# Kernel optimization log

Measured on AMD Instinct MI355X. Metric: run time of the kernel, lower is better.

The kernel has to match this reference:

```python
import jax, jax.numpy as jnp
import numpy as np

C = 8.0  # RG-LRU temporal-gate constant (Griffin paper, c = 8)


def setup_inputs() -> dict:
    key = jax.random.key(0)
    ks = jax.random.split(key, 4)
    S, B, D = 2048, 8, 2048  # (seq_len, batch, width); batch_first=False layout
    s = 1.0 / np.sqrt(D).astype(np.float32)
    return {
        "x": jax.random.normal(ks[0], (S, B, D), jnp.float32),
        "h0": jnp.zeros((B, D), jnp.float32),
        "W_x": jax.random.normal(ks[1], (D, D), jnp.float32) * s,
        "b_x": jnp.zeros((D,), jnp.float32),
        "W_a": jax.random.normal(ks[2], (D, D), jnp.float32) * s,
        "b_a": jnp.zeros((D,), jnp.float32),
        "a_param": jax.random.uniform(ks[3], (D,), jnp.float32, 0.3, 1.0),
    }


def _rg_lru(x, h0, W_x, b_x, W_a, b_a, a_param):
    # x: (S, B, D) time-major. RG-LRU (Griffin/Hawk), num_heads=1 so the
    # block-diagonal gate projections are plain dense D->D linears.
    S = x.shape[0]
    gate_x = jax.nn.sigmoid(jnp.einsum("sbd,ed->sbe", x, W_x) + b_x)  # input gate
    gate_a = jax.nn.sigmoid(jnp.einsum("sbd,ed->sbe", x, W_a) + b_a)  # recurrence gate
    log_a = -C * gate_a * jax.nn.softplus(a_param)  # (S, B, D), log of decay in (0,1)
    a = jnp.exp(log_a)
    multiplier = jnp.sqrt(1.0 - jnp.exp(2.0 * log_a))  # sqrt(1 - a^2) normalizer
    # Reset at segment start (t == 0): multiplier -> 1, decay -> 0 (cache cleared).
    reset = (jnp.arange(S) == 0)[:, None, None]
    multiplier = jnp.where(reset, 1.0, multiplier)
    a = jnp.where(reset, 0.0, a)
    normed_x = x * gate_x * multiplier  # gated, variance-normalized input

    def step(h, inp):
        a_t, x_t = inp
        h = a_t * h + x_t  # diagonal linear recurrence
        return h, h

    hn, y = jax.lax.scan(step, h0, (a, normed_x))
    return y, hn  # y: (S, B, D) since batch_first=False; hn: (B, D)


def reference(x, h0, W_x, b_x, W_a, b_a, a_param):
    return _rg_lru(x, h0, W_x, b_x, W_a, b_a, a_param)
```

## Files before the change

kernel.cpp:

```cpp
#include <hip/hip_runtime.h>
#include <cstdint>

#define S_LEN 2048
#define B_SZ 8
#define D_DIM 2048
#define M_DIM (S_LEN * B_SZ)
#define CHAINS (B_SZ * D_DIM)
#define BK 64
#define KTILES (D_DIM / BK)

typedef __bf16 bf16;
typedef bf16 bf16x8 __attribute__((ext_vector_type(8)));
typedef bf16 bf16x4 __attribute__((ext_vector_type(4)));
typedef float f32x4 __attribute__((ext_vector_type(4)));

__device__ __forceinline__ void async_copy16(void* lds, const void* g) {
    __builtin_amdgcn_global_load_lds(
        (const __attribute__((address_space(1))) unsigned int*)g,
        (__attribute__((address_space(3))) unsigned int*)lds,
        16, 0, 0);
}

__global__ void k_convert(const float4* __restrict__ x,
                          const float4* __restrict__ wx,
                          const float4* __restrict__ wa,
                          bf16* __restrict__ xb,
                          bf16* __restrict__ wi) {
    const long NX4 = (long)M_DIM * D_DIM / 4;
    const long NW4 = (long)D_DIM * D_DIM / 4;
    const long total = NX4 + 2 * NW4;
    for (long i = (long)blockIdx.x * blockDim.x + threadIdx.x; i < total;
         i += (long)gridDim.x * blockDim.x) {
        float4 v;
        bf16* dst;
        if (i < NX4) {
            v = x[i];
            dst = xb + 4 * i;
        } else {
            long k = i - NX4;
            const int isA = k >= NW4;
            if (isA) k -= NW4;
            const long e = k >> 9;
            const long col4 = k & 511;
            const long drow = (e >> 4) * 32 + (isA ? 16 : 0) + (e & 15);
            v = (isA ? wa : wx)[k];
            dst = wi + (drow * 512 + col4) * 4;
        }
        bf16x4 o;
        o[0] = (bf16)v.x; o[1] = (bf16)v.y; o[2] = (bf16)v.z; o[3] = (bf16)v.w;
        *reinterpret_cast<bf16x4*>(dst) = o;
    }
}

__global__ void k_cvec(const float* __restrict__ ap, float* __restrict__ cv) {
    int e = blockIdx.x * blockDim.x + threadIdx.x;
    if (e < D_DIM) {
        float v = ap[e];
        cv[e] = -8.0f * log1pf(expf(v));
    }
}

__global__ __launch_bounds__(512, 2) void k_gemm(
    const bf16* __restrict__ xb,
    const bf16* __restrict__ wi,
    const float* __restrict__ x32,
    const float* __restrict__ bx,
    const float* __restrict__ ba,
    const float* __restrict__ cv,
    float* __restrict__ abuf,
    float* __restrict__ y)
{
    __shared__ __align__(16) char smem[131072];

    const int tid  = threadIdx.x;
    const int lane = tid & 63;
    const int w    = tid >> 6;
    const int wm   = w >> 2;
    const int wn   = w & 3;

    const int orig = blockIdx.x;
    const int wgid = (orig & 7) * 128 + (orig >> 3);
    const int m0 = (wgid & 63) * 256;
    const int e0 = (wgid >> 6) * 256;

    const int srow  = lane >> 3;
    const int swz16 = ((lane & 7) ^ srow) * 16;

    const char* gA = (const char*)xb;
    const char* gB = (const char*)wi;

#define STAGE_A(buf, kt) do {                                                  \
    const long kb_ = (long)(kt) * 128 + swz16;                                 \
    _Pragma("unroll")                                                          \
    for (int j_ = 0; j_ < 4; ++j_) {                                           \
        const int br_ = w * 32 + j_ * 8;                                       \
        async_copy16(smem + (buf) * 65536 + br_ * 128,                         \
                     gA + ((long)(m0 + br_ + srow) * 4096 + kb_));             \
    } } while (0)

#define STAGE_B(buf, kt) do {                                                  \
    const long kb_ = (long)(kt) * 128 + swz16;                                 \
    _Pragma("unroll")                                                          \
    for (int j_ = 0; j_ < 4; ++j_) {                                           \
        const int br_ = w * 32 + j_ * 8;                                       \
        async_copy16(smem + (buf) * 65536 + 32768 + br_ * 128,                 \
                     gB + ((long)(e0 + br_ + srow) * 4096 + kb_));             \
    } } while (0)

#define PHASE_MID() do {                                                       \
    __builtin_amdgcn_s_barrier();                                              \
    asm volatile("s_waitcnt lgkmcnt(0)" ::: "memory");                         \
    __builtin_amdgcn_sched_barrier(0);                                         \
    __builtin_amdgcn_s_setprio(1); } while (0)

#define PHASE_END() do {                                                       \
    __builtin_amdgcn_s_setprio(0);                                             \
    __builtin_amdgcn_s_barrier(); } while (0)

    f32x4 acc[8][4];
#pragma unroll
    for (int i = 0; i < 8; ++i)
#pragma unroll
        for (int j = 0; j < 4; ++j) acc[i][j] = (f32x4)(0.0f);

    STAGE_A(0, 0); STAGE_B(0, 0);
    asm volatile("s_waitcnt vmcnt(0)" ::: "memory");
    __builtin_amdgcn_s_barrier();

    const int rL = lane & 15;

    for (int kt = 0; kt < KTILES; ++kt) {
        const int c  = kt & 1;
        const int nb = 1 - c;
        char* sA = smem + c * 65536;
        char* sB = sA + 32768;
        const bool pf = (kt < KTILES - 1);

        bf16x8 af[4], bf[4];

#define LOAD_AF(ihalf, ks) do {                                                \
    _Pragma("unroll")                                                          \
    for (int i_ = 0; i_ < 4; ++i_) {                                           \
        const int r_ = wm * 128 + ((ihalf) * 4 + i_) * 16 + rL;                \
        const int ch_ = (((ks) * 4 + (lane >> 4)) ^ (r_ & 7)) * 16;            \
        af[i_] = *reinterpret_cast<const bf16x8*>(sA + r_ * 128 + ch_);        \
    } } while (0)

#define LOAD_BF(ks) do {                                                       \
    _Pragma("unroll")                                                          \
    for (int j_ = 0; j_ < 4; ++j_) {                                           \
        const int r_ = wn * 64 + j_ * 16 + rL;                                 \
        const int ch_ = (((ks) * 4 + (lane >> 4)) ^ (r_ & 7)) * 16;            \
        bf[j_] = *reinterpret_cast<const bf16x8*>(sB + r_ * 128 + ch_);        \
    } } while (0)

#define MFMA16(ihalf) do {                                                     \
    _Pragma("unroll")                                                          \
    for (int i_ = 0; i_ < 4; ++i_)                                             \
        _Pragma("unroll")                                                      \
        for (int j_ = 0; j_ < 4; ++j_)                                         \
            acc[(ihalf) * 4 + i_][j_] = __builtin_amdgcn_mfma_f32_16x16x32_bf16( \
                af[i_], bf[j_], acc[(ihalf) * 4 + i_][j_], 0, 0, 0);           \
    } while (0)

        LOAD_BF(0); LOAD_AF(0, 0);
        if (pf) STAGE_A(nb, kt + 1);
        PHASE_MID(); MFMA16(0); PHASE_END();

        LOAD_AF(1, 0);
        if (pf) STAGE_B(nb, kt + 1);
        PHASE_MID(); MFMA16(1); PHASE_END();

        LOAD_BF(1); LOAD_AF(0, 1);
        PHASE_MID(); MFMA16(0); PHASE_END();

        LOAD_AF(1, 1);
        PHASE_MID(); MFMA16(1);
        __builtin_amdgcn_s_setprio(0);
        if (pf) asm volatile("s_waitcnt vmcnt(0)" ::: "memory");
        __builtin_amdgcn_s_barrier();

#undef LOAD_AF
#undef LOAD_BF
#undef MFMA16
    }

#undef STAGE_A
#undef STAGE_B
#undef PHASE_MID
#undef PHASE_END

    const int rgrp = lane >> 4;
    const int chb  = (e0 + wn * 64) >> 1;
#pragma unroll
    for (int jj = 0; jj < 2; ++jj) {
        const int ch = chb + jj * 16 + rL;
        const float bxv = bx[ch];
        const float bav = ba[ch];
        const float cvv = cv[ch];
#pragma unroll
        for (int i = 0; i < 8; ++i) {
#pragma unroll
            for (int r = 0; r < 4; ++r) {
                const int m = m0 + wm * 128 + i * 16 + rgrp * 4 + r;
                const float zx = acc[i][2 * jj][r] + bxv;
                const float za = acc[i][2 * jj + 1][r] + bav;
                const float gx = 1.0f / (1.0f + __expf(-zx));
                const float ga = 1.0f / (1.0f + __expf(-za));
                const float la = cvv * ga;
                float a = __expf(la);
                float mult = sqrtf(fmaxf(1.0f - a * a, 0.0f));
                if (m < B_SZ) { a = 0.0f; mult = 1.0f; }
                const long o = (long)m * D_DIM + ch;
                const float xv = x32[o];
                abuf[o] = a;
                y[o] = xv * gx * mult;
            }
        }
    }
}

__global__ __launch_bounds__(64) void k_scan(
    const float* __restrict__ abuf,
    float* __restrict__ y,
    const float* __restrict__ h0,
    float* __restrict__ hn) {
    const int c = blockIdx.x * 64 + threadIdx.x;
    float h = h0[c];

    float av0[16], xv0[16], av1[16], xv1[16];
#pragma unroll
    for (int j = 0; j < 16; ++j) {
        const long o = (long)j * CHAINS + c;
        av0[j] = abuf[o];
        xv0[j] = y[o];
    }
    for (int g = 0; g < 128; g += 2) {
        const long base1 = ((long)(g + 1) * 16) * CHAINS + c;
        if (g + 1 < 128) {
#pragma unroll
            for (int j = 0; j < 16; ++j) {
                av1[j] = abuf[base1 + (long)j * CHAINS];
                xv1[j] = y[base1 + (long)j * CHAINS];
            }
        }
        const long base0 = ((long)g * 16) * CHAINS + c;
#pragma unroll
        for (int j = 0; j < 16; ++j) {
            h = fmaf(av0[j], h, xv0[j]);
            y[base0 + (long)j * CHAINS] = h;
        }
        const long base2 = ((long)(g + 2) * 16) * CHAINS + c;
        if (g + 2 < 128) {
#pragma unroll
            for (int j = 0; j < 16; ++j) {
                av0[j] = abuf[base2 + (long)j * CHAINS];
                xv0[j] = y[base2 + (long)j * CHAINS];
            }
        }
        if (g + 1 < 128) {
#pragma unroll
            for (int j = 0; j < 16; ++j) {
                h = fmaf(av1[j], h, xv1[j]);
                y[base1 + (long)j * CHAINS] = h;
            }
        }
    }
    hn[c] = h;
}

extern "C" void kernel_launch(void* const* d_in, const int* in_sizes, int n_in,
                              void* d_out, int out_size, void* d_ws, size_t ws_size,
                              hipStream_t stream) {
    const float* x  = (const float*)d_in[0];
    const float* h0 = (const float*)d_in[1];
    const float* Wx = (const float*)d_in[2];
    const float* bx = (const float*)d_in[3];
    const float* Wa = (const float*)d_in[4];
    const float* ba = (const float*)d_in[5];
    const float* ap = (const float*)d_in[6];
    float* out = (float*)d_out;

    char* ws = (char*)d_ws;
    bf16*  xb   = (bf16*)(ws);
    bf16*  wi   = (bf16*)(ws + 67108864L);
    float* cv   = (float*)(ws + 83886080L);
    float* abuf = (float*)(ws + 83894272L);

    float* y  = out;
    float* hn = out + (long)M_DIM * D_DIM;

    k_convert<<<dim3(2048), dim3(256), 0, stream>>>(
        (const float4*)x, (const float4*)Wx, (const float4*)Wa, xb, wi);
    k_cvec<<<dim3(8), dim3(256), 0, stream>>>(ap, cv);
    k_gemm<<<dim3((M_DIM / 256) * (2 * D_DIM / 256)), dim3(512), 0, stream>>>(
        xb, wi, x, bx, ba, cv, abuf, y);
    k_scan<<<dim3(CHAINS / 64), dim3(64), 0, stream>>>(abuf, y, h0, hn);
}
```

Baseline: 488.3 us.

## Pack log-decay and normed input as bf16 pair; drop intra-phase barriers

The GEMM epilogue now packs log(a) and the normalized input into one 32-bit word (two bf16 halves), written to a workspace buffer. It reads x from the bf16 copy instead of fp32, and it no longer writes the fp32 a-buffer and y separately. The scan reads a single 4-byte word per step and recomputes exp(log a), which roughly halves the intermediate traffic between GEMM and scan. The GEMM main loop also drops the per-phase s_barriers and keeps only the end-of-tile barrier. The costs are reduced precision (bf16 for both log-decay and input) and possible wave desynchronization in the MFMA loop.

```diff
diff --git a/kernel.cpp b/kernel.cpp
--- a/kernel.cpp
+++ b/kernel.cpp
@@ -19,6 +19,11 @@
         (const __attribute__((address_space(1))) unsigned int*)g,
         (__attribute__((address_space(3))) unsigned int*)lds,
         16, 0, 0);
+}
+
+__device__ __forceinline__ unsigned short bf16_bits(float f) {
+    bf16 b = (bf16)f;
+    return __builtin_bit_cast(unsigned short, b);
 }
 
 __global__ void k_convert(const float4* __restrict__ x,
@@ -63,12 +68,10 @@
 __global__ __launch_bounds__(512, 2) void k_gemm(
     const bf16* __restrict__ xb,
     const bf16* __restrict__ wi,
-    const float* __restrict__ x32,
     const float* __restrict__ bx,
     const float* __restrict__ ba,
     const float* __restrict__ cv,
-    float* __restrict__ abuf,
-    float* __restrict__ y)
+    unsigned int* __restrict__ pk)
 {
     __shared__ __align__(16) char smem[131072];
 
@@ -107,15 +110,11 @@
                      gB + ((long)(e0 + br_ + srow) * 4096 + kb_));             \
     } } while (0)
 
-#define PHASE_MID() do {                                                       \
-    __builtin_amdgcn_s_barrier();                                              \
+#define PHASE_GO() do {                                                        \
     asm volatile("s_waitcnt lgkmcnt(0)" ::: "memory");                         \
     __builtin_amdgcn_sched_barrier(0);                                         \
     __builtin_amdgcn_s_setprio(1); } while (0)
-
-#define PHASE_END() do {                                                       \
-    __builtin_amdgcn_s_setprio(0);                                             \
-    __builtin_amdgcn_s_barrier(); } while (0)
+#define PHASE_DONE() __builtin_amdgcn_s_setprio(0)
 
     f32x4 acc[8][4];
 #pragma unroll
@@ -165,18 +164,18 @@
 
         LOAD_BF(0); LOAD_AF(0, 0);
         if (pf) STAGE_A(nb, kt + 1);
-        PHASE_MID(); MFMA16(0); PHASE_END();
+        PHASE_GO(); MFMA16(0); PHASE_DONE();
 
         LOAD_AF(1, 0);
         if (pf) STAGE_B(nb, kt + 1);
-        PHASE_MID(); MFMA16(1); PHASE_END();
+        PHASE_GO(); MFMA16(1); PHASE_DONE();
 
         LOAD_BF(1); LOAD_AF(0, 1);
-        PHASE_MID(); MFMA16(0); PHASE_END();
+        PHASE_GO(); MFMA16(0); PHASE_DONE();
 
         LOAD_AF(1, 1);
-        PHASE_MID(); MFMA16(1);
-        __builtin_amdgcn_s_setprio(0);
+        PHASE_GO(); MFMA16(1); PHASE_DONE();
+
         if (pf) asm volatile("s_waitcnt vmcnt(0)" ::: "memory");
         __builtin_amdgcn_s_barrier();
 
@@ -187,8 +186,8 @@
 
 #undef STAGE_A
 #undef STAGE_B
-#undef PHASE_MID
-#undef PHASE_END
+#undef PHASE_GO
+#undef PHASE_DONE
 
     const int rgrp = lane >> 4;
     const int chb  = (e0 + wn * 64) >> 1;
@@ -207,61 +206,59 @@
                 const float za = acc[i][2 * jj + 1][r] + bav;
                 const float gx = 1.0f / (1.0f + __expf(-zx));
                 const float ga = 1.0f / (1.0f + __expf(-za));
-                const float la = cvv * ga;
-                float a = __expf(la);
-                float mult = sqrtf(fmaxf(1.0f - a * a, 0.0f));
-                if (m < B_SZ) { a = 0.0f; mult = 1.0f; }
+                float la = cvv * ga;
+                float mult = sqrtf(fmaxf(1.0f - __expf(2.0f * la), 0.0f));
+                if (m < B_SZ) { la = -100.0f; mult = 1.0f; }
                 const long o = (long)m * D_DIM + ch;
-                const float xv = x32[o];
-                abuf[o] = a;
-                y[o] = xv * gx * mult;
+                const float xv = (float)xb[o];
+                const float xn = xv * gx * mult;
+                const unsigned int u =
+                    ((unsigned int)bf16_bits(xn) << 16) | bf16_bits(la);
+                pk[o] = u;
             }
         }
     }
 }
 
 __global__ __launch_bounds__(64) void k_scan(
-    const float* __restrict__ abuf,
+    const unsigned int* __restrict__ pk,
     float* __restrict__ y,
     const float* __restrict__ h0,
     float* __restrict__ hn) {
     const int c = blockIdx.x * 64 + threadIdx.x;
     float h = h0[c];
 
-    float av0[16], xv0[16], av1[16], xv1[16];
-#pragma unroll
-    for (int j = 0; j < 16; ++j) {
-        const long o = (long)j * CHAINS + c;
-        av0[j] = abuf[o];
-        xv0[j] = y[o];
-    }
+    unsigned int u0[16], u1[16];
+#pragma unroll
+    for (int j = 0; j < 16; ++j) u0[j] = pk[(long)j * CHAINS + c];
+
     for (int g = 0; g < 128; g += 2) {
         const long base1 = ((long)(g + 1) * 16) * CHAINS + c;
         if (g + 1 < 128) {
 #pragma unroll
-            for (int j = 0; j < 16; ++j) {
-                av1[j] = abuf[base1 + (long)j * CHAINS];
-                xv1[j] = y[base1 + (long)j * CHAINS];
-            }
+            for (int j = 0; j < 16; ++j) u1[j] = pk[base1 + (long)j * CHAINS];
         }
         const long base0 = ((long)g * 16) * CHAINS + c;
 #pragma unroll
         for (int j = 0; j < 16; ++j) {
-            h = fmaf(av0[j], h, xv0[j]);
+            const unsigned int u = u0[j];
+            const float la = __builtin_bit_cast(float, u << 16);
+            const float xn = __builtin_bit_cast(float, u & 0xffff0000u);
+            h = fmaf(__expf(la), h, xn);
             y[base0 + (long)j * CHAINS] = h;
         }
         const long base2 = ((long)(g + 2) * 16) * CHAINS + c;
         if (g + 2 < 128) {
 #pragma unroll
+            for (int j = 0; j < 16; ++j) u0[j] = pk[base2 + (long)j * CHAINS];
+        }
+        if (g + 1 < 128) {
+#pragma unroll
             for (int j = 0; j < 16; ++j) {
-                av0[j] = abuf[base2 + (long)j * CHAINS];
-                xv0[j] = y[base2 + (long)j * CHAINS];
-            }
-        }
-        if (g + 1 < 128) {
-#pragma unroll
-            for (int j = 0; j < 16; ++j) {
-                h = fmaf(av1[j], h, xv1[j]);
+                const unsigned int u = u1[j];
+                const float la = __builtin_bit_cast(float, u << 16);
+                const float xn = __builtin_bit_cast(float, u & 0xffff0000u);
+                h = fmaf(__expf(la), h, xn);
                 y[base1 + (long)j * CHAINS] = h;
             }
         }
@@ -282,10 +279,10 @@
     float* out = (float*)d_out;
 
     char* ws = (char*)d_ws;
-    bf16*  xb   = (bf16*)(ws);
-    bf16*  wi   = (bf16*)(ws + 67108864L);
-    float* cv   = (float*)(ws + 83886080L);
-    float* abuf = (float*)(ws + 83894272L);
+    bf16*  xb = (bf16*)(ws);
+    bf16*  wi = (bf16*)(ws + 67108864L);
+    float* cv = (float*)(ws + 83886080L);
+    unsigned int* pk = (unsigned int*)(ws + 83894272L);
 
     float* y  = out;
     float* hn = out + (long)M_DIM * D_DIM;
@@ -294,6 +291,6 @@
         (const float4*)x, (const float4*)Wx, (const float4*)Wa, xb, wi);
     k_cvec<<<dim3(8), dim3(256), 0, stream>>>(ap, cv);
     k_gemm<<<dim3((M_DIM / 256) * (2 * D_DIM / 256)), dim3(512), 0, stream>>>(
-        xb, wi, x, bx, ba, cv, abuf, y);
-    k_scan<<<dim3(CHAINS / 64), dim3(64), 0, stream>>>(abuf, y, h0, hn);
-}
+        xb, wi, bx, ba, cv, pk);
+    k_scan<<<dim3(CHAINS / 64), dim3(64), 0, stream>>>(pk, y, h0, hn);
+}
```

After: 418.1 us. 14.4% less time.
